# Kernel tuning notes

Measured on AMD Instinct MI355X. Metric: run time of the kernel, lower is better.

## Reference

```python
import jax, jax.numpy as jnp
import numpy as np

# xxh32 primes
_P1 = jnp.uint32(2654435761)
_P2 = jnp.uint32(2246822519)
_P3 = jnp.uint32(3266489917)
_P4 = jnp.uint32(668265263)
_P5 = jnp.uint32(374761393)


def _rotl32(v, r):
    r = jnp.uint32(r)
    return (v << r) | (v >> (jnp.uint32(32) - r))


def xxh32_4bytes(val_u32, seed_u32):
    """xxh32 of a single 4-byte (little-endian) input, fully vectorized.

    Matches xxhash.xxh32(struct.pack('<I', val), seed).intdigest().
    """
    acc = seed_u32 + _P5 + jnp.uint32(4)          # seed + PRIME5 + length
    acc = acc + val_u32 * _P3                      # consume one 4-byte lane
    acc = _rotl32(acc, 17) * _P4
    # avalanche
    acc = acc ^ (acc >> jnp.uint32(15))
    acc = acc * _P2
    acc = acc ^ (acc >> jnp.uint32(13))
    acc = acc * _P3
    acc = acc ^ (acc >> jnp.uint32(16))
    return acc


EMB_LEVELS = 1_000_000
EMB_DIM = 64
N = 16384
F = 20


def setup_inputs() -> dict:
    key = jax.random.key(0)
    k1, k2, k3 = jax.random.split(key, 3)
    x = jax.random.randint(k1, (N,), 0, 2147483647, dtype=jnp.int32)
    fnum = jax.random.randint(k2, (F,), 0, 100000, dtype=jnp.int32)
    emb = jax.random.normal(k3, (EMB_LEVELS, EMB_DIM), dtype=jnp.float32)
    return {"x": x, "fnum": fnum, "emb": emb}


def reference(x, fnum, emb):
    # hash every (row, seed) pair in parallel: [N, 1] x [1, F] -> [N, F]
    val = x.astype(jnp.uint32)[:, None]
    seed = fnum.astype(jnp.uint32)[None, :]
    h = xxh32_4bytes(val, seed)                      # uint32 [N, F]
    idx = (h % jnp.uint32(emb.shape[0])).astype(jnp.int32)
    out = emb[idx]                                   # [N, F, D] gather
    return out.reshape(x.shape[0], -1)               # [N, F*D]
```

## Files before the change

### kernel.cpp

```cpp
#include <hip/hip_runtime.h>
#include <stdint.h>

#define XP2 2246822519u
#define XP3 3266489917u
#define XP4 668265263u
#define XP5 374761393u

constexpr int EMB_LEVELS = 1000000;
constexpr int F = 20;

__device__ __forceinline__ uint32_t rotl32(uint32_t v, int r) {
    return (v << r) | (v >> (32 - r));
}

__global__ __launch_bounds__(256) void ue_kernel(
    const int* __restrict__ x,
    const int* __restrict__ fnum,
    const float4* __restrict__ emb,
    float4* __restrict__ out,
    int total_pairs)
{
    int t    = blockIdx.x * blockDim.x + threadIdx.x;
    int pair = t >> 4;
    int lane = t & 15;
    if (pair >= total_pairs) return;

    int n = pair / F;
    int f = pair - n * F;

    uint32_t val  = (uint32_t)x[n];
    uint32_t seed = (uint32_t)fnum[f];

    uint32_t acc = seed + XP5 + 4u;
    acc += val * XP3;
    acc = rotl32(acc, 17) * XP4;
    acc ^= acc >> 15;
    acc *= XP2;
    acc ^= acc >> 13;
    acc *= XP3;
    acc ^= acc >> 16;

    uint32_t idx = acc % (uint32_t)EMB_LEVELS;

    out[(size_t)pair * 16 + lane] = emb[(size_t)idx * 16 + lane];
}

extern "C" void kernel_launch(void* const* d_in, const int* in_sizes, int n_in,
                              void* d_out, int out_size, void* d_ws, size_t ws_size,
                              hipStream_t stream) {
    const int*   x    = (const int*)d_in[0];
    const int*   fnum = (const int*)d_in[1];
    const float* emb  = (const float*)d_in[2];
    float*       out  = (float*)d_out;

    int n_rows = in_sizes[0];
    int total_pairs = n_rows * F;
    int total_threads = total_pairs * 16;
    int block = 256;
    int grid = (total_threads + block - 1) / block;

    ue_kernel<<<grid, block, 0, stream>>>(
        x, fnum, (const float4*)emb, (float4*)out, total_pairs);
}
```

Measured before the change: 331.8 us.

## Use grid-stride loop with 4-way batched gathers and nontemporal output stores

Replaces the one-thread-per-float4 launch with a fixed 2560-block grid-stride loop. Each thread issues four independent embedding gathers before storing any of them, which raises memory-level parallelism. Output writes use nontemporal stores so the 84 MB streaming output does not pollute the cache. The risk is that the fixed grid size does not suit the device, and the extra loop and predicate overhead could offset the gain.

```diff
diff --git a/kernel.cpp b/kernel.cpp
--- a/kernel.cpp
+++ b/kernel.cpp
@@ -8,29 +8,15 @@
 
 constexpr int EMB_LEVELS = 1000000;
 constexpr int F = 20;
+constexpr int UNROLL = 4;
+
+typedef float f32x4 __attribute__((ext_vector_type(4)));
 
 __device__ __forceinline__ uint32_t rotl32(uint32_t v, int r) {
     return (v << r) | (v >> (32 - r));
 }
 
-__global__ __launch_bounds__(256) void ue_kernel(
-    const int* __restrict__ x,
-    const int* __restrict__ fnum,
-    const float4* __restrict__ emb,
-    float4* __restrict__ out,
-    int total_pairs)
-{
-    int t    = blockIdx.x * blockDim.x + threadIdx.x;
-    int pair = t >> 4;
-    int lane = t & 15;
-    if (pair >= total_pairs) return;
-
-    int n = pair / F;
-    int f = pair - n * F;
-
-    uint32_t val  = (uint32_t)x[n];
-    uint32_t seed = (uint32_t)fnum[f];
-
+__device__ __forceinline__ uint32_t xxh32_4(uint32_t val, uint32_t seed) {
     uint32_t acc = seed + XP5 + 4u;
     acc += val * XP3;
     acc = rotl32(acc, 17) * XP4;
@@ -39,10 +25,47 @@
     acc ^= acc >> 13;
     acc *= XP3;
     acc ^= acc >> 16;
+    return acc;
+}
 
-    uint32_t idx = acc % (uint32_t)EMB_LEVELS;
+__global__ __launch_bounds__(256) void ue_kernel(
+    const int* __restrict__ x,
+    const int* __restrict__ fnum,
+    const f32x4* __restrict__ emb,
+    f32x4* __restrict__ out,
+    int total_units)
+{
+    const int stride = gridDim.x * blockDim.x;
+    const int t0 = blockIdx.x * blockDim.x + threadIdx.x;
 
-    out[(size_t)pair * 16 + lane] = emb[(size_t)idx * 16 + lane];
+    for (int base = t0; base < total_units; base += stride * UNROLL) {
+        f32x4 v[UNROLL];
+        int   tu[UNROLL];
+        bool  ok[UNROLL];
+
+        #pragma unroll
+        for (int u = 0; u < UNROLL; u++) {
+            int t = base + u * stride;
+            ok[u] = (t < total_units);
+            tu[u] = t;
+            if (ok[u]) {
+                int pair = t >> 4;
+                int lane = t & 15;
+                int n = pair / F;
+                int f = pair - n * F;
+                uint32_t h = xxh32_4((uint32_t)x[n], (uint32_t)fnum[f]);
+                uint32_t idx = h % (uint32_t)EMB_LEVELS;
+                v[u] = emb[(size_t)idx * 16 + lane];
+            }
+        }
+
+        #pragma unroll
+        for (int u = 0; u < UNROLL; u++) {
+            if (ok[u]) {
+                __builtin_nontemporal_store(v[u], &out[(size_t)tu[u]]);
+            }
+        }
+    }
 }
 
 extern "C" void kernel_launch(void* const* d_in, const int* in_sizes, int n_in,
@@ -55,10 +78,11 @@
 
     int n_rows = in_sizes[0];
     int total_pairs = n_rows * F;
-    int total_threads = total_pairs * 16;
+    int total_units = total_pairs * 16;
+
     int block = 256;
-    int grid = (total_threads + block - 1) / block;
+    int grid  = 2560;
 
     ue_kernel<<<grid, block, 0, stream>>>(
-        x, fnum, (const float4*)emb, (float4*)out, total_pairs);
+        x, fnum, (const f32x4*)emb, (f32x4*)out, total_units);
 }
```

Result: no change. 334.6 us (+0.8%).
